# Optimization experiments

Hardware: AMD Instinct MI355X
Metric: run time of the kernel (lower is better)

The kernel has to match this reference:

```python
import jax, jax.numpy as jnp
import numpy as np

N, C_IN, C_RED, H, W = 16, 256, 64, 48, 48


def conv1x1(x, w, b):
    # x: [N, Cin, H, W], w: [Cout, Cin], b: [Cout]
    return jnp.einsum('nchw,oc->nohw', x, w) + b[None, :, None, None]


def setup_inputs() -> dict:
    key = jax.random.key(0)
    ks = jax.random.split(key, 10)
    s_in = 1.0 / np.sqrt(C_IN)
    s_red = 1.0 / np.sqrt(C_RED)
    return {
        'feature_maps': jax.random.normal(ks[0], (N, C_IN, H, W), jnp.float32),
        'global_channel_output': jax.random.normal(ks[1], (N, C_IN, H, W), jnp.float32),
        'Wq': jax.random.uniform(ks[2], (C_RED, C_IN), jnp.float32, -s_in, s_in),
        'bq': jax.random.uniform(ks[3], (C_RED,), jnp.float32, -s_in, s_in),
        'Wk': jax.random.uniform(ks[4], (C_RED, C_IN), jnp.float32, -s_in, s_in),
        'bk': jax.random.uniform(ks[5], (C_RED,), jnp.float32, -s_in, s_in),
        'Wv': jax.random.uniform(ks[6], (C_RED, C_IN), jnp.float32, -s_in, s_in),
        'bv': jax.random.uniform(ks[7], (C_RED,), jnp.float32, -s_in, s_in),
        'Watt': jax.random.uniform(ks[8], (C_IN, C_RED), jnp.float32, -s_red, s_red),
        'batt': jax.random.uniform(ks[9], (C_IN,), jnp.float32, -s_red, s_red),
    }


def reference(feature_maps, global_channel_output, Wq, bq, Wk, bk, Wv, bv, Watt, batt):
    n, _, h, w = feature_maps.shape
    hw = h * w
    q = conv1x1(feature_maps, Wq, bq).reshape(n, -1, hw)   # [N, Cr, HW]
    k = conv1x1(feature_maps, Wk, bk).reshape(n, -1, hw)   # [N, Cr, HW]
    v = conv1x1(feature_maps, Wv, bv).reshape(n, -1, hw)   # [N, Cr, HW]
    # key^T @ query -> [N, HW, HW]
    qk = jnp.einsum('nci,ncj->nij', k, q)
    # global (flattened) softmax over the whole HWxHW matrix per batch element
    qk = jax.nn.softmax(qk.reshape(n, hw * hw), axis=-1).reshape(n, hw, hw)
    att = jnp.einsum('nci,nij->ncj', v, qk).reshape(n, -1, h, w)  # [N, Cr, H, W]
    att = conv1x1(att, Watt, batt)                                 # [N, Cin, H, W]
    return global_channel_output * att + global_channel_output
```

## Files before the change

kernel.cpp:

```cpp
#include <hip/hip_runtime.h>
#include <hip/hip_bf16.h>
#include <stdint.h>

#define NB   16
#define CIN  256
#define CRED 64
#define HW   2304
#define NJT  36
#define NIG  2
#define NIT  18

typedef __bf16 bf16;
typedef __bf16 bf16x8 __attribute__((ext_vector_type(8)));
typedef __bf16 bf16x4 __attribute__((ext_vector_type(4)));
typedef float  f32x4  __attribute__((ext_vector_type(4)));

__global__ __launch_bounds__(256) void qkv_kernel(
    const float* __restrict__ x,
    const float* __restrict__ Wq, const float* __restrict__ bq,
    const float* __restrict__ Wk, const float* __restrict__ bk,
    const float* __restrict__ Wv, const float* __restrict__ bv,
    bf16* __restrict__ qT, bf16* __restrict__ kT, bf16* __restrict__ v)
{
    __shared__ __align__(16) bf16 sX[32 * 264];
    const int jt = blockIdx.x, n = blockIdx.y;
    const int jbase = jt * 32;
    const int tid = threadIdx.x;
    const int lane = tid & 63, w = tid >> 6;
    const int l15 = lane & 15, q4 = lane >> 4;

    const float* xn = x + ((size_t)n * CIN) * HW + jbase;
    #pragma unroll
    for (int it = 0; it < 8; ++it) {
        int idx = tid + 256 * it;
        int c = idx >> 3, p4 = idx & 7;
        const float4 vv = *(const float4*)(xn + c * HW + p4 * 4);
        sX[(p4 * 4 + 0) * 264 + c] = (bf16)vv.x;
        sX[(p4 * 4 + 1) * 264 + c] = (bf16)vv.y;
        sX[(p4 * 4 + 2) * 264 + c] = (bf16)vv.z;
        sX[(p4 * 4 + 3) * 264 + c] = (bf16)vv.w;
    }
    __syncthreads();

    const float* Ws[3] = {Wq, Wk, Wv};
    const float* bs[3] = {bq, bk, bv};
    #pragma unroll
    for (int wi = 0; wi < 3; ++wi) {
        bf16x8 a[8];
        const float* Wp = Ws[wi] + (w * 16 + l15) * CIN + q4 * 8;
        #pragma unroll
        for (int ks = 0; ks < 8; ++ks) {
            float4 f0 = *(const float4*)(Wp + ks * 32);
            float4 f1 = *(const float4*)(Wp + ks * 32 + 4);
            bf16x8 t = {(bf16)f0.x, (bf16)f0.y, (bf16)f0.z, (bf16)f0.w,
                        (bf16)f1.x, (bf16)f1.y, (bf16)f1.z, (bf16)f1.w};
            a[ks] = t;
        }
        f32x4 acc[2] = {};
        #pragma unroll
        for (int nt = 0; nt < 2; ++nt) {
            #pragma unroll
            for (int ks = 0; ks < 8; ++ks) {
                bf16x8 b = *(const bf16x8*)(sX + (nt * 16 + l15) * 264 + ks * 32 + q4 * 8);
                acc[nt] = __builtin_amdgcn_mfma_f32_16x16x32_bf16(a[ks], b, acc[nt], 0, 0, 0);
            }
        }
        const int crb = w * 16 + q4 * 4;
        const float b0 = bs[wi][crb], b1 = bs[wi][crb + 1],
                    b2 = bs[wi][crb + 2], b3 = bs[wi][crb + 3];
        if (wi < 2) {
            bf16* dst = (wi == 0 ? qT : kT) + ((size_t)n * HW) * 64;
            #pragma unroll
            for (int nt = 0; nt < 2; ++nt) {
                int pos = jbase + nt * 16 + l15;
                bf16x4 pk = {(bf16)(acc[nt].x + b0), (bf16)(acc[nt].y + b1),
                             (bf16)(acc[nt].z + b2), (bf16)(acc[nt].w + b3)};
                *(bf16x4*)(dst + pos * 64 + crb) = pk;
            }
        } else {
            bf16* dst = v + ((size_t)n * CRED) * HW;
            #pragma unroll
            for (int nt = 0; nt < 2; ++nt) {
                int pos = jbase + nt * 16 + l15;
                dst[(crb + 0) * HW + pos] = (bf16)(acc[nt].x + b0);
                dst[(crb + 1) * HW + pos] = (bf16)(acc[nt].y + b1);
                dst[(crb + 2) * HW + pos] = (bf16)(acc[nt].z + b2);
                dst[(crb + 3) * HW + pos] = (bf16)(acc[nt].w + b3);
            }
        }
    }
}

__global__ __launch_bounds__(256, 5) void attn_kernel(
    const bf16* __restrict__ qT, const bf16* __restrict__ kT,
    const bf16* __restrict__ v,
    float* __restrict__ OTp, float* __restrict__ Z)
{
    __shared__ __align__(16) bf16 sQP[64 * 72];
    __shared__ __align__(16) bf16 sK[64 * 72];
    __shared__ __align__(16) bf16 sV[64 * 72];
    const int jt = blockIdx.x, ig = blockIdx.y, n = blockIdx.z;
    const int jbase = jt * 64;
    const int tid = threadIdx.x;
    const int lane = tid & 63, w = tid >> 6;
    const int l15 = lane & 15, q4 = lane >> 4;

    {
        const uint4* src = (const uint4*)(qT + ((size_t)n * HW + jbase) * 64);
        uint4* dst = (uint4*)sQP;
        for (int i = tid; i < 512; i += 256) {
            int r = i >> 3, c = i & 7;
            dst[r * 9 + c] = src[r * 8 + c];
        }
    }
    __syncthreads();
    bf16x8 qf[4][2];
    #pragma unroll
    for (int nt = 0; nt < 4; ++nt)
        #pragma unroll
        for (int ks = 0; ks < 2; ++ks)
            qf[nt][ks] = *(const bf16x8*)(sQP + (nt * 16 + l15) * 72 + ks * 32 + q4 * 8);

    f32x4 oacc[4] = {};
    float zacc = 0.f;
    const uint4* ksrc = (const uint4*)(kT + ((size_t)n * HW) * 64);
    const bf16* vbase = v + ((size_t)n * CRED) * HW;

    for (int it = 0; it < NIT; ++it) {
        const int ibase = (ig * NIT + it) * 64;
        __syncthreads();
        {
            uint4* dk = (uint4*)sK;
            uint4* dv = (uint4*)sV;
            const uint4* sk = ksrc + ibase * 8;
            for (int i = tid; i < 512; i += 256) {
                int r = i >> 3, c = i & 7;
                dk[r * 9 + c] = sk[r * 8 + c];
                dv[r * 9 + c] = *(const uint4*)(vbase + r * HW + ibase + c * 8);
            }
        }
        __syncthreads();
        bf16x8 kf0 = *(const bf16x8*)(sK + (w * 16 + l15) * 72 + 0 * 32 + q4 * 8);
        bf16x8 kf1 = *(const bf16x8*)(sK + (w * 16 + l15) * 72 + 1 * 32 + q4 * 8);
        #pragma unroll
        for (int nt = 0; nt < 4; ++nt) {
            f32x4 accs = {};
            accs = __builtin_amdgcn_mfma_f32_16x16x32_bf16(kf0, qf[nt][0], accs, 0, 0, 0);
            accs = __builtin_amdgcn_mfma_f32_16x16x32_bf16(kf1, qf[nt][1], accs, 0, 0, 0);
            float p0 = __expf(accs.x), p1 = __expf(accs.y);
            float p2 = __expf(accs.z), p3 = __expf(accs.w);
            zacc += (p0 + p1) + (p2 + p3);
            bf16x4 pk = {(bf16)p0, (bf16)p1, (bf16)p2, (bf16)p3};
            *(bf16x4*)(sQP + (nt * 16 + l15) * 72 + w * 16 + q4 * 4) = pk;
        }
        __syncthreads();
        bf16x8 vf0 = *(const bf16x8*)(sV + (w * 16 + l15) * 72 + 0 * 32 + q4 * 8);
        bf16x8 vf1 = *(const bf16x8*)(sV + (w * 16 + l15) * 72 + 1 * 32 + q4 * 8);
        #pragma unroll
        for (int nt = 0; nt < 4; ++nt) {
            bf16x8 p0 = *(const bf16x8*)(sQP + (nt * 16 + l15) * 72 + 0 * 32 + q4 * 8);
            bf16x8 p1 = *(const bf16x8*)(sQP + (nt * 16 + l15) * 72 + 1 * 32 + q4 * 8);
            oacc[nt] = __builtin_amdgcn_mfma_f32_16x16x32_bf16(vf0, p0, oacc[nt], 0, 0, 0);
            oacc[nt] = __builtin_amdgcn_mfma_f32_16x16x32_bf16(vf1, p1, oacc[nt], 0, 0, 0);
        }
    }
    float* OTn = OTp + (((size_t)ig * NB + n) * HW) * 64;
    #pragma unroll
    for (int nt = 0; nt < 4; ++nt) {
        int pos = jbase + nt * 16 + l15;
        *(f32x4*)(OTn + pos * 64 + w * 16 + q4 * 4) = oacc[nt];
    }
    #pragma unroll
    for (int off = 32; off > 0; off >>= 1) zacc += __shfl_down(zacc, off);
    if (lane == 0) atomicAdd(Z + n, zacc);
}

__global__ __launch_bounds__(256) void out_kernel(
    const float* __restrict__ OTp, const float* __restrict__ Z,
    const float* __restrict__ Watt, const float* __restrict__ batt,
    const float* __restrict__ g, float* __restrict__ out)
{
    __shared__ __align__(16) bf16 sO[16 * 72];
    const int jt = blockIdx.x, n = blockIdx.y;
    const int jbase = jt * 16;
    const int tid = threadIdx.x;
    const int lane = tid & 63, w = tid >> 6;
    const int l15 = lane & 15, q4 = lane >> 4;
    const float invZ = 1.0f / Z[n];

    {
        int r = tid >> 4, c4 = tid & 15;
        const float* p = OTp + (((size_t)n * HW) + jbase + r) * 64 + c4 * 4;
        float4 v0 = *(const float4*)(p);
        float4 v1 = *(const float4*)(p + (size_t)NB * HW * 64);
        bf16x4 pk = {(bf16)((v0.x + v1.x) * invZ),
                     (bf16)((v0.y + v1.y) * invZ),
                     (bf16)((v0.z + v1.z) * invZ),
                     (bf16)((v0.w + v1.w) * invZ)};
        *(bf16x4*)(sO + r * 72 + c4 * 4) = pk;
    }
    __syncthreads();

    const float* gp = g + ((size_t)n * CIN) * HW;
    float* op = out + ((size_t)n * CIN) * HW;
    bf16x8 b0 = *(const bf16x8*)(sO + l15 * 72 + 0 * 32 + q4 * 8);
    bf16x8 b1 = *(const bf16x8*)(sO + l15 * 72 + 1 * 32 + q4 * 8);
    #pragma unroll
    for (int mt = 0; mt < 4; ++mt) {
        const float* Wp = Watt + (w * 64 + mt * 16 + l15) * 64 + q4 * 8;
        float4 f0 = *(const float4*)(Wp);
        float4 f1 = *(const float4*)(Wp + 4);
        float4 f2 = *(const float4*)(Wp + 32);
        float4 f3 = *(const float4*)(Wp + 36);
        bf16x8 a0 = {(bf16)f0.x, (bf16)f0.y, (bf16)f0.z, (bf16)f0.w,
                     (bf16)f1.x, (bf16)f1.y, (bf16)f1.z, (bf16)f1.w};
        bf16x8 a1 = {(bf16)f2.x, (bf16)f2.y, (bf16)f2.z, (bf16)f2.w,
                     (bf16)f3.x, (bf16)f3.y, (bf16)f3.z, (bf16)f3.w};
        f32x4 acc = {};
        acc = __builtin_amdgcn_mfma_f32_16x16x32_bf16(a0, b0, acc, 0, 0, 0);
        acc = __builtin_amdgcn_mfma_f32_16x16x32_bf16(a1, b1, acc, 0, 0, 0);
        const int co = w * 64 + mt * 16 + q4 * 4;
        const int pos = jbase + l15;
        const float c0 = batt[co], c1 = batt[co + 1], c2 = batt[co + 2], c3 = batt[co + 3];
        const float g0 = gp[(co + 0) * HW + pos], g1 = gp[(co + 1) * HW + pos];
        const float g2 = gp[(co + 2) * HW + pos], g3 = gp[(co + 3) * HW + pos];
        op[(co + 0) * HW + pos] = g0 * (acc.x + c0 + 1.0f);
        op[(co + 1) * HW + pos] = g1 * (acc.y + c1 + 1.0f);
        op[(co + 2) * HW + pos] = g2 * (acc.z + c2 + 1.0f);
        op[(co + 3) * HW + pos] = g3 * (acc.w + c3 + 1.0f);
    }
}

extern "C" void kernel_launch(void* const* d_in, const int* in_sizes, int n_in,
                              void* d_out, int out_size, void* d_ws, size_t ws_size,
                              hipStream_t stream) {
    const float* x    = (const float*)d_in[0];
    const float* g    = (const float*)d_in[1];
    const float* Wq   = (const float*)d_in[2];
    const float* bq   = (const float*)d_in[3];
    const float* Wk   = (const float*)d_in[4];
    const float* bk   = (const float*)d_in[5];
    const float* Wv   = (const float*)d_in[6];
    const float* bv   = (const float*)d_in[7];
    const float* Watt = (const float*)d_in[8];
    const float* batt = (const float*)d_in[9];
    float* out = (float*)d_out;

    char* ws = (char*)d_ws;
    const size_t qkv_sz = (size_t)NB * HW * CRED * sizeof(bf16);
    bf16*  qT = (bf16*)(ws);
    bf16*  kT = (bf16*)(ws + qkv_sz);
    bf16*  vv = (bf16*)(ws + 2 * qkv_sz);
    float* OTp = (float*)(ws + 3 * qkv_sz);
    float* Z  = (float*)(ws + 3 * qkv_sz + (size_t)NIG * NB * HW * CRED * sizeof(float));

    hipMemsetAsync(Z, 0, NB * sizeof(float), stream);

    dim3 blk(256);
    qkv_kernel<<<dim3(HW / 32, NB), blk, 0, stream>>>(x, Wq, bq, Wk, bk, Wv, bv, qT, kT, vv);
    attn_kernel<<<dim3(NJT, NIG, NB), blk, 0, stream>>>(qT, kT, vv, OTp, Z);
    out_kernel<<<dim3(HW / 16, NB), blk, 0, stream>>>(OTp, Z, Watt, batt, g, out);
}
```

Before: 276.0 us.

## Prefetch K/V tiles in registers, pre-convert weights, use exp2 with scaled Q

Adds a prep kernel that converts all weights to bf16 once and folds log2(e) into Wq and bq, so the attention softmax can use exp2f instead of __expf. The attention loop now holds the next K/V tile in registers and stores it to shared memory at the start of the following iteration, overlapping global loads with MFMA work; the occupancy hint drops from 5 to 4 blocks. The output kernel handles 64 positions per block and reuses the weight fragments across four column tiles. The cost is one extra kernel launch and more register pressure in the attention loop.

```diff
diff --git a/kernel.cpp b/kernel.cpp
--- a/kernel.cpp
+++ b/kernel.cpp
@@ -15,11 +15,27 @@
 typedef __bf16 bf16x4 __attribute__((ext_vector_type(4)));
 typedef float  f32x4  __attribute__((ext_vector_type(4)));
 
+__global__ __launch_bounds__(256) void prep_kernel(
+    const float* __restrict__ Wq, const float* __restrict__ bq,
+    const float* __restrict__ Wk, const float* __restrict__ Wv,
+    const float* __restrict__ Watt,
+    bf16* __restrict__ Wqb, bf16* __restrict__ Wkb, bf16* __restrict__ Wvb,
+    bf16* __restrict__ Wab, float* __restrict__ bqs)
+{
+    const float INVLN2 = 1.44269504088896f;
+    int i = blockIdx.x * 256 + threadIdx.x;
+    Wqb[i] = (bf16)(Wq[i] * INVLN2);
+    Wkb[i] = (bf16)Wk[i];
+    Wvb[i] = (bf16)Wv[i];
+    Wab[i] = (bf16)Watt[i];
+    if (i < CRED) bqs[i] = bq[i] * INVLN2;
+}
+
 __global__ __launch_bounds__(256) void qkv_kernel(
     const float* __restrict__ x,
-    const float* __restrict__ Wq, const float* __restrict__ bq,
-    const float* __restrict__ Wk, const float* __restrict__ bk,
-    const float* __restrict__ Wv, const float* __restrict__ bv,
+    const bf16* __restrict__ Wqb, const float* __restrict__ bqs,
+    const bf16* __restrict__ Wkb, const float* __restrict__ bk,
+    const bf16* __restrict__ Wvb, const float* __restrict__ bv,
     bf16* __restrict__ qT, bf16* __restrict__ kT, bf16* __restrict__ v)
 {
     __shared__ __align__(16) bf16 sX[32 * 264];
@@ -42,20 +58,14 @@
     }
     __syncthreads();
 
-    const float* Ws[3] = {Wq, Wk, Wv};
-    const float* bs[3] = {bq, bk, bv};
+    const bf16*  Ws[3] = {Wqb, Wkb, Wvb};
+    const float* bs[3] = {bqs, bk, bv};
     #pragma unroll
     for (int wi = 0; wi < 3; ++wi) {
         bf16x8 a[8];
-        const float* Wp = Ws[wi] + (w * 16 + l15) * CIN + q4 * 8;
-        #pragma unroll
-        for (int ks = 0; ks < 8; ++ks) {
-            float4 f0 = *(const float4*)(Wp + ks * 32);
-            float4 f1 = *(const float4*)(Wp + ks * 32 + 4);
-            bf16x8 t = {(bf16)f0.x, (bf16)f0.y, (bf16)f0.z, (bf16)f0.w,
-                        (bf16)f1.x, (bf16)f1.y, (bf16)f1.z, (bf16)f1.w};
-            a[ks] = t;
-        }
+        const bf16* Wp = Ws[wi] + (w * 16 + l15) * CIN + q4 * 8;
+        #pragma unroll
+        for (int ks = 0; ks < 8; ++ks) a[ks] = *(const bf16x8*)(Wp + ks * 32);
         f32x4 acc[2] = {};
         #pragma unroll
         for (int nt = 0; nt < 2; ++nt) {
@@ -91,7 +101,7 @@
     }
 }
 
-__global__ __launch_bounds__(256, 5) void attn_kernel(
+__global__ __launch_bounds__(256, 4) void attn_kernel(
     const bf16* __restrict__ qT, const bf16* __restrict__ kT,
     const bf16* __restrict__ v,
     float* __restrict__ OTp, float* __restrict__ Z)
@@ -126,20 +136,31 @@
     const uint4* ksrc = (const uint4*)(kT + ((size_t)n * HW) * 64);
     const bf16* vbase = v + ((size_t)n * CRED) * HW;
 
+    const int r0 = tid >> 3, c0 = tid & 7;
+    const int ibase0 = ig * NIT * 64;
+
+    uint4 kr0 = ksrc[(ibase0 + r0) * 8 + c0];
+    uint4 kr1 = ksrc[(ibase0 + r0 + 32) * 8 + c0];
+    uint4 vr0 = *(const uint4*)(vbase + (size_t)r0 * HW + ibase0 + c0 * 8);
+    uint4 vr1 = *(const uint4*)(vbase + (size_t)(r0 + 32) * HW + ibase0 + c0 * 8);
+
+    uint4* dk = (uint4*)sK;
+    uint4* dv = (uint4*)sV;
+
     for (int it = 0; it < NIT; ++it) {
-        const int ibase = (ig * NIT + it) * 64;
+        const int ibase = ibase0 + it * 64;
         __syncthreads();
-        {
-            uint4* dk = (uint4*)sK;
-            uint4* dv = (uint4*)sV;
-            const uint4* sk = ksrc + ibase * 8;
-            for (int i = tid; i < 512; i += 256) {
-                int r = i >> 3, c = i & 7;
-                dk[r * 9 + c] = sk[r * 8 + c];
-                dv[r * 9 + c] = *(const uint4*)(vbase + r * HW + ibase + c * 8);
-            }
-        }
+        dk[r0 * 9 + c0] = kr0;
+        dk[(r0 + 32) * 9 + c0] = kr1;
+        dv[r0 * 9 + c0] = vr0;
+        dv[(r0 + 32) * 9 + c0] = vr1;
+        const int nbase = (it + 1 < NIT) ? ibase + 64 : ibase;
+        kr0 = ksrc[(nbase + r0) * 8 + c0];
+        kr1 = ksrc[(nbase + r0 + 32) * 8 + c0];
+        vr0 = *(const uint4*)(vbase + (size_t)r0 * HW + nbase + c0 * 8);
+        vr1 = *(const uint4*)(vbase + (size_t)(r0 + 32) * HW + nbase + c0 * 8);
         __syncthreads();
+
         bf16x8 kf0 = *(const bf16x8*)(sK + (w * 16 + l15) * 72 + 0 * 32 + q4 * 8);
         bf16x8 kf1 = *(const bf16x8*)(sK + (w * 16 + l15) * 72 + 1 * 32 + q4 * 8);
         #pragma unroll
@@ -147,8 +168,8 @@
             f32x4 accs = {};
             accs = __builtin_amdgcn_mfma_f32_16x16x32_bf16(kf0, qf[nt][0], accs, 0, 0, 0);
             accs = __builtin_amdgcn_mfma_f32_16x16x32_bf16(kf1, qf[nt][1], accs, 0, 0, 0);
-            float p0 = __expf(accs.x), p1 = __expf(accs.y);
-            float p2 = __expf(accs.z), p3 = __expf(accs.w);
+            float p0 = exp2f(accs.x), p1 = exp2f(accs.y);
+            float p2 = exp2f(accs.z), p3 = exp2f(accs.w);
             zacc += (p0 + p1) + (p2 + p3);
             bf16x4 pk = {(bf16)p0, (bf16)p1, (bf16)p2, (bf16)p3};
             *(bf16x4*)(sQP + (nt * 16 + l15) * 72 + w * 16 + q4 * 4) = pk;
@@ -177,19 +198,19 @@
 
 __global__ __launch_bounds__(256) void out_kernel(
     const float* __restrict__ OTp, const float* __restrict__ Z,
-    const float* __restrict__ Watt, const float* __restrict__ batt,
+    const bf16* __restrict__ Wab, const float* __restrict__ batt,
     const float* __restrict__ g, float* __restrict__ out)
 {
-    __shared__ __align__(16) bf16 sO[16 * 72];
+    __shared__ __align__(16) bf16 sO[64 * 72];
     const int jt = blockIdx.x, n = blockIdx.y;
-    const int jbase = jt * 16;
+    const int jbase = jt * 64;
     const int tid = threadIdx.x;
     const int lane = tid & 63, w = tid >> 6;
     const int l15 = lane & 15, q4 = lane >> 4;
     const float invZ = 1.0f / Z[n];
 
-    {
-        int r = tid >> 4, c4 = tid & 15;
+    for (int i = tid; i < 1024; i += 256) {
+        int r = i >> 4, c4 = i & 15;
         const float* p = OTp + (((size_t)n * HW) + jbase + r) * 64 + c4 * 4;
         float4 v0 = *(const float4*)(p);
         float4 v1 = *(const float4*)(p + (size_t)NB * HW * 64);
@@ -201,33 +222,35 @@
     }
     __syncthreads();
 
+    bf16x8 bfr[4][2];
+    #pragma unroll
+    for (int nt = 0; nt < 4; ++nt)
+        #pragma unroll
+        for (int ks = 0; ks < 2; ++ks)
+            bfr[nt][ks] = *(const bf16x8*)(sO + (nt * 16 + l15) * 72 + ks * 32 + q4 * 8);
+
     const float* gp = g + ((size_t)n * CIN) * HW;
     float* op = out + ((size_t)n * CIN) * HW;
-    bf16x8 b0 = *(const bf16x8*)(sO + l15 * 72 + 0 * 32 + q4 * 8);
-    bf16x8 b1 = *(const bf16x8*)(sO + l15 * 72 + 1 * 32 + q4 * 8);
     #pragma unroll
     for (int mt = 0; mt < 4; ++mt) {
-        const float* Wp = Watt + (w * 64 + mt * 16 + l15) * 64 + q4 * 8;
-        float4 f0 = *(const float4*)(Wp);
-        float4 f1 = *(const float4*)(Wp + 4);
-        float4 f2 = *(const float4*)(Wp + 32);
-        float4 f3 = *(const float4*)(Wp + 36);
-        bf16x8 a0 = {(bf16)f0.x, (bf16)f0.y, (bf16)f0.z, (bf16)f0.w,
-                     (bf16)f1.x, (bf16)f1.y, (bf16)f1.z, (bf16)f1.w};
-        bf16x8 a1 = {(bf16)f2.x, (bf16)f2.y, (bf16)f2.z, (bf16)f2.w,
-                     (bf16)f3.x, (bf16)f3.y, (bf16)f3.z, (bf16)f3.w};
-        f32x4 acc = {};
-        acc = __builtin_amdgcn_mfma_f32_16x16x32_bf16(a0, b0, acc, 0, 0, 0);
-        acc = __builtin_amdgcn_mfma_f32_16x16x32_bf16(a1, b1, acc, 0, 0, 0);
+        const bf16* Wp = Wab + (w * 64 + mt * 16 + l15) * 64 + q4 * 8;
+        bf16x8 a0 = *(const bf16x8*)(Wp);
+        bf16x8 a1 = *(const bf16x8*)(Wp + 32);
         const int co = w * 64 + mt * 16 + q4 * 4;
-        const int pos = jbase + l15;
         const float c0 = batt[co], c1 = batt[co + 1], c2 = batt[co + 2], c3 = batt[co + 3];
-        const float g0 = gp[(co + 0) * HW + pos], g1 = gp[(co + 1) * HW + pos];
-        const float g2 = gp[(co + 2) * HW + pos], g3 = gp[(co + 3) * HW + pos];
-        op[(co + 0) * HW + pos] = g0 * (acc.x + c0 + 1.0f);
-        op[(co + 1) * HW + pos] = g1 * (acc.y + c1 + 1.0f);
-        op[(co + 2) * HW + pos] = g2 * (acc.z + c2 + 1.0f);
-        op[(co + 3) * HW + pos] = g3 * (acc.w + c3 + 1.0f);
+        #pragma unroll
+        for (int nt = 0; nt < 4; ++nt) {
+            f32x4 acc = {};
+            acc = __builtin_amdgcn_mfma_f32_16x16x32_bf16(a0, bfr[nt][0], acc, 0, 0, 0);
+            acc = __builtin_amdgcn_mfma_f32_16x16x32_bf16(a1, bfr[nt][1], acc, 0, 0, 0);
+            const int pos = jbase + nt * 16 + l15;
+            const float g0 = gp[(co + 0) * HW + pos], g1 = gp[(co + 1) * HW + pos];
+            const float g2 = gp[(co + 2) * HW + pos], g3 = gp[(co + 3) * HW + pos];
+            op[(co + 0) * HW + pos] = g0 * (acc.x + c0 + 1.0f);
+            op[(co + 1) * HW + pos] = g1 * (acc.y + c1 + 1.0f);
+            op[(co + 2) * HW + pos] = g2 * (acc.z + c2 + 1.0f);
+            op[(co + 3) * HW + pos] = g3 * (acc.w + c3 + 1.0f);
+        }
     }
 }
 
@@ -248,16 +271,23 @@
 
     char* ws = (char*)d_ws;
     const size_t qkv_sz = (size_t)NB * HW * CRED * sizeof(bf16);
-    bf16*  qT = (bf16*)(ws);
-    bf16*  kT = (bf16*)(ws + qkv_sz);
-    bf16*  vv = (bf16*)(ws + 2 * qkv_sz);
+    bf16*  qT  = (bf16*)(ws);
+    bf16*  kT  = (bf16*)(ws + qkv_sz);
+    bf16*  vv  = (bf16*)(ws + 2 * qkv_sz);
     float* OTp = (float*)(ws + 3 * qkv_sz);
-    float* Z  = (float*)(ws + 3 * qkv_sz + (size_t)NIG * NB * HW * CRED * sizeof(float));
-
-    hipMemsetAsync(Z, 0, NB * sizeof(float), stream);
+    char*  w2  = ws + 3 * qkv_sz + (size_t)NIG * NB * HW * CRED * sizeof(float);
+    float* Zp  = (float*)(w2);
+    bf16*  Wqb = (bf16*)(w2 + 256);
+    bf16*  Wkb = Wqb + CRED * CIN;
+    bf16*  Wvb = Wkb + CRED * CIN;
+    bf16*  Wab = Wvb + CRED * CIN;
+    float* bqs = (float*)(Wab + CIN * CRED);
+
+    hipMemsetAsync(Zp, 0, NB * sizeof(float), stream);
 
     dim3 blk(256);
-    qkv_kernel<<<dim3(HW / 32, NB), blk, 0, stream>>>(x, Wq, bq, Wk, bk, Wv, bv, qT, kT, vv);
-    attn_kernel<<<dim3(NJT, NIG, NB), blk, 0, stream>>>(qT, kT, vv, OTp, Z);
-    out_kernel<<<dim3(HW / 16, NB), blk, 0, stream>>>(OTp, Z, Watt, batt, g, out);
-}
+    prep_kernel<<<dim3(64), blk, 0, stream>>>(Wq, bq, Wk, Wv, Watt, Wqb, Wkb, Wvb, Wab, bqs);
+    qkv_kernel<<<dim3(HW / 32, NB), blk, 0, stream>>>(x, Wqb, bqs, Wkb, bk, Wvb, bv, qT, kT, vv);
+    attn_kernel<<<dim3(NJT, NIG, NB), blk, 0, stream>>>(qT, kT, vv, OTp, Zp);
+    out_kernel<<<dim3(NJT, NB), blk, 0, stream>>>(OTp, Zp, Wab, batt, g, out);
+}
```

Result: faster. 251.4 us (-8.9%).
